# Kernel optimization log

Hardware: AMD Instinct MI355X
Metric: run time of the kernel (lower is better)

## Reference

```python
import jax, jax.numpy as jnp
import numpy as np

K = 64          # number of tags, incl. BOS/EOS
V = 50000       # vocab size (excl. BOS/EOS words)
D = 128         # lexicon embedding dim
BOS_T = K - 2   # BOS tag index
EOS_T = K - 1   # EOS tag index
BATCH = 8192
L = 126         # interior words per sentence (n = L + 2 incl. BOS/EOS)
EPS = 1e-45     # smoothing added to A and B in updateAB


def setup_inputs() -> dict:
    key = jax.random.key(0)
    k1, k2, k3, k4 = jax.random.split(key, 4)
    words = jax.random.randint(k1, (BATCH, L), 0, V, dtype=jnp.int32)
    ThetaB = 0.01 * jax.random.uniform(k2, (K, D), dtype=jnp.float32)
    WA = 0.01 * jax.random.uniform(k3, (K, K), dtype=jnp.float32)
    E = jax.random.normal(k4, (V, D), dtype=jnp.float32)
    return {"words": words, "ThetaB": ThetaB, "WA": WA, "E": E}


def reference(words, ThetaB, WA, E):
    # updateAB(): A = softmax(WA) with BOS column forced to prob 0 (-inf logit)
    WAm = WA.at[:, BOS_T].set(-jnp.inf)
    A = jax.nn.softmax(WAm, axis=1) + EPS                       # [K, K]
    B = jax.nn.softmax(ThetaB @ E.T, axis=1)                    # [K, V]
    B = B.at[EOS_T, :].set(0.0).at[BOS_T, :].set(0.0) + EPS
    logA = jnp.log(A)                                           # [K, K]
    logB = jnp.log(B)                                           # [K, V]

    # Emission log-probs gathered per token: [L, B, K]
    em = jnp.swapaxes(logB.T[words], 0, 1)

    # alpha_0: one-hot (in log space) at BOS tag
    alpha0 = jnp.full((words.shape[0], K), -jnp.inf, dtype=logA.dtype)
    alpha0 = alpha0.at[:, BOS_T].set(0.0)

    def step(alpha, e):
        # alpha: [B, K] over prev tags; logsumexp over prev tag axis
        new = jax.nn.logsumexp(alpha[:, :, None] + logA[None, :, :], axis=1) + e
        return new, None

    alpha, _ = jax.lax.scan(step, alpha0, em)
    # Final transition into EOS tag (no emission): log Z per sentence, [B]
    logZ = jax.nn.logsumexp(alpha + logA[None, :, EOS_T], axis=1)
    return logZ
```

## Files before the change

kernel.cpp:

```cpp
#include <hip/hip_runtime.h>
#include <hip/hip_bf16.h>
#include <math.h>


#define KT 64
#define VV 50000
#define DD 128
#define BOS_T 62
#define EOS_T 63
#define LLEN 126
#define EPSF 1e-45f
#define SCALE_F 65536.0f
#define LOG_TOTAL_SCALE (2016.0f * 0.6931471805599453f)
#define NBLK 782
#define PBLK 784
#define TPH 14
#define NPH 9

#define BTN_OFF   0
#define A_OFF     6400000
#define SUM_OFF   6416384
#define PART_OFF  6416640

typedef short short8 __attribute__((ext_vector_type(8)));
typedef float f32x4  __attribute__((ext_vector_type(4)));

union U8 { short8 v; unsigned u[4]; short s[8]; };

static __device__ inline unsigned short f2bf_u(float x) {
    __hip_bfloat16 h = __float2bfloat16(x);
    return *reinterpret_cast<unsigned short*>(&h);
}
static __device__ inline short f2bf(float x) { return (short)f2bf_u(x); }

#if __has_builtin(__builtin_amdgcn_cvt_pk_bf16_f32)
typedef __bf16 bf16x2 __attribute__((ext_vector_type(2)));
static __device__ inline unsigned pk2(float a, float b) {
    bf16x2 r = __builtin_amdgcn_cvt_pk_bf16_f32(a, b);
    return *reinterpret_cast<unsigned*>(&r);
}
#else
static __device__ inline unsigned pk2(float a, float b) {
    union { float f; unsigned u; } ua, ub;
    ua.f = a; ub.f = b;
    return ((ua.u + 0x8000u) >> 16) | ((ub.u + 0x8000u) & 0xFFFF0000u);
}
#endif
static __device__ inline float lo16(unsigned u) { union { unsigned i; float f; } c; c.i = u << 16;        return c.f; }
static __device__ inline float hi16(unsigned u) { union { unsigned i; float f; } c; c.i = u & 0xffff0000u; return c.f; }

#if __has_builtin(__builtin_amdgcn_global_load_lds)
#define GLLDS(gp, lbase)                                                        \
    __builtin_amdgcn_global_load_lds(                                           \
        (__attribute__((address_space(1))) void*)const_cast<unsigned short*>(gp),\
        (__attribute__((address_space(3))) void*)(lbase), 16, 0, 0)
#else
#define GLLDS(gp, lbase)                                                        \
    do { *(uint4*)((unsigned short*)(lbase) + (threadIdx.x & 63) * 8) =         \
             *(const uint4*)(gp); } while (0)
#endif

__global__ __launch_bounds__(256) void k_emit(const float* __restrict__ ThetaB,
                                              const float* __restrict__ E,
                                              unsigned short* __restrict__ btn_bf,
                                              float* __restrict__ partial) {
    __shared__ float red[4][KT];
    int t    = threadIdx.x;
    int lane = t & 63;
    int w    = t >> 6;
    int n    = lane & 15;
    int q    = lane >> 4;
    int v0   = (blockIdx.x * 4 + w) * 16;

    int rowE = v0 + n;
    bool valid = rowE < VV;
    rowE = valid ? rowE : VV - 1;
    float4 ex[4][2];
#pragma unroll
    for (int kt = 0; kt < 4; ++kt) {
        const float* p = E + (size_t)rowE * DD + kt * 32 + q * 8;
        ex[kt][0] = *(const float4*)p;
        ex[kt][1] = *(const float4*)(p + 4);
    }

    short8 Th[4][4];
#pragma unroll
    for (int kt = 0; kt < 4; ++kt)
#pragma unroll
        for (int mt = 0; mt < 4; ++mt) {
            const float* p = ThetaB + (mt * 16 + n) * DD + kt * 32 + q * 8;
            float4 x = *(const float4*)p;
            float4 y = *(const float4*)(p + 4);
            U8 f;
            f.u[0] = pk2(x.x, x.y); f.u[1] = pk2(x.z, x.w);
            f.u[2] = pk2(y.x, y.y); f.u[3] = pk2(y.z, y.w);
            Th[kt][mt] = f.v;
        }

    short8 Ef[4];
#pragma unroll
    for (int kt = 0; kt < 4; ++kt) {
        U8 f;
        f.u[0] = pk2(ex[kt][0].x, ex[kt][0].y); f.u[1] = pk2(ex[kt][0].z, ex[kt][0].w);
        f.u[2] = pk2(ex[kt][1].x, ex[kt][1].y); f.u[3] = pk2(ex[kt][1].z, ex[kt][1].w);
        Ef[kt] = f.v;
    }

#pragma unroll
    for (int mt = 0; mt < 4; ++mt) {
        f32x4 C = {0.f, 0.f, 0.f, 0.f};
#pragma unroll
        for (int kt = 0; kt < 4; ++kt)
            C = __builtin_amdgcn_mfma_f32_16x16x32_bf16(Th[kt][mt], Ef[kt], C, 0, 0, 0);
        float e[4];
#pragma unroll
        for (int r = 0; r < 4; ++r) e[r] = __expf(C[r]);
        if (valid) {
            uint2 st = make_uint2(pk2(e[0], e[1]), pk2(e[2], e[3]));
            *(uint2*)(btn_bf + (size_t)rowE * KT + mt * 16 + q * 4) = st;
        }
#pragma unroll
        for (int r = 0; r < 4; ++r) {
            float s = valid ? e[r] : 0.0f;
            s += __shfl_xor(s, 1, 64);
            s += __shfl_xor(s, 2, 64);
            s += __shfl_xor(s, 4, 64);
            s += __shfl_xor(s, 8, 64);
            if (n == 0) red[w][mt * 16 + q * 4 + r] = s;
        }
    }
    __syncthreads();
    if (w == 0) {
        float s = red[0][lane] + red[1][lane] + red[2][lane] + red[3][lane];
        partial[lane * PBLK + blockIdx.x] = s;
    }
}

__global__ __launch_bounds__(256) void k_sumA(const float* __restrict__ partial,
                                              const float* __restrict__ WA,
                                              float* __restrict__ sumexp,
                                              float* __restrict__ A) {
    __shared__ float r[4];
    int k = blockIdx.x;
    int t = threadIdx.x;
    float s = 0.0f;
    for (int i = t; i < NBLK; i += 256) s += partial[k * PBLK + i];
#pragma unroll
    for (int off = 32; off > 0; off >>= 1) s += __shfl_xor(s, off, 64);
    if ((t & 63) == 0) r[t >> 6] = s;
    __syncthreads();
    if (t == 0) sumexp[k] = r[0] + r[1] + r[2] + r[3];
    if (t < 64) {
        float wv = WA[k * KT + t];
        float e = (t == BOS_T) ? 0.0f : __expf(wv);
        float se = e;
#pragma unroll
        for (int off = 32; off > 0; off >>= 1) se += __shfl_xor(se, off, 64);
        A[k * KT + t] = e / se + EPSF;
    }
}

__global__ __launch_bounds__(64) void k_fwd(const int* __restrict__ words,
                                            const unsigned short* __restrict__ btn_bf,
                                            const float* __restrict__ A,
                                            const float* __restrict__ sumexp,
                                            float* __restrict__ out) {
    __shared__ int shw[16 * LLEN];
    __shared__ __attribute__((aligned(16))) unsigned short shE[2][TPH * 1024];
    int lane = threadIdx.x & 63;
    int n    = lane & 15;
    int qA   = lane >> 4;
    int b0   = blockIdx.x * 16;

    {
        const uint4* src = (const uint4*)(words + (size_t)b0 * LLEN);
        uint4* dst = (uint4*)shw;
#pragma unroll
        for (int i = 0; i < 8; ++i) {
            int idx = lane + 64 * i;
            if (idx < (16 * LLEN) / 4) dst[idx] = src[idx];
        }
    }

    short8 Af[2][4];
#pragma unroll
    for (int mt = 0; mt < 4; ++mt) {
        int tagn = 32 * (mt >> 1) + 8 * (n >> 2) + 4 * (mt & 1) + (n & 3);
        float s = sumexp[tagn];
        float rsn = (tagn == BOS_T || tagn == EOS_T) ? 0.0f : (SCALE_F / s);
#pragma unroll
        for (int kt = 0; kt < 2; ++kt) {
            U8 f;
#pragma unroll
            for (int j = 0; j < 8; ++j)
                f.s[j] = f2bf(A[(kt * 32 + qA * 8 + j) * KT + tagn] * rsn);
            Af[kt][mt] = f.v;
        }
    }

    short8 B0, B1;
    {
        U8 z; z.u[0] = z.u[1] = z.u[2] = z.u[3] = 0;
        B0 = z.v;
        U8 o; o.u[0] = o.u[1] = o.u[2] = o.u[3] = 0;
        if (qA == 3) o.s[6] = (short)0x3F80;
        B1 = o.v;
    }

#define STAGE(bb, t0)                                                        \
    do {                                                                     \
        _Pragma("unroll")                                                    \
        for (int s_ = 0; s_ < TPH; ++s_) {                                   \
            int wd_ = shw[n * LLEN + (t0) + s_];                             \
            const unsigned short* g_ = btn_bf + (size_t)wd_ * KT + qA * 8;   \
            GLLDS(g_, &shE[bb][s_ * 1024]);                                  \
            GLLDS(g_ + 32, &shE[bb][s_ * 1024 + 512]);                       \
        }                                                                    \
    } while (0)

#define LDE(bb, ss, hh) (*(const uint4*)(&shE[bb][(ss) * 1024 + (hh) * 512] + lane * 8))

    STAGE(0, 0);
    asm volatile("s_waitcnt vmcnt(0)" ::: "memory");

    for (int p = 0; p < NPH; ++p) {
        int b = p & 1;
        if (p + 1 < NPH) STAGE((p + 1) & 1, (p + 1) * TPH);

        uint4 a0 = LDE(b, 0, 0), a1 = LDE(b, 0, 1);
        uint4 c0 = LDE(b, 1, 0), c1 = LDE(b, 1, 1);
#pragma unroll
        for (int s = 0; s < TPH; ++s) {
            uint4 e0 = a0, e1 = a1;
            a0 = c0; a1 = c1;
            int s2 = (s + 2 < TPH) ? s + 2 : TPH - 1;
            c0 = LDE(b, s2, 0); c1 = LDE(b, s2, 1);

            f32x4 C[4];
#pragma unroll
            for (int mt = 0; mt < 4; ++mt) {
                f32x4 acc = {0.f, 0.f, 0.f, 0.f};
                acc = __builtin_amdgcn_mfma_f32_16x16x32_bf16(Af[0][mt], B0, acc, 0, 0, 0);
                acc = __builtin_amdgcn_mfma_f32_16x16x32_bf16(Af[1][mt], B1, acc, 0, 0, 0);
                C[mt] = acc;
            }
            U8 f0, f1;
            f0.u[0] = pk2(C[0][0] * lo16(e0.x), C[0][1] * hi16(e0.x));
            f0.u[1] = pk2(C[0][2] * lo16(e0.y), C[0][3] * hi16(e0.y));
            f0.u[2] = pk2(C[1][0] * lo16(e0.z), C[1][1] * hi16(e0.z));
            f0.u[3] = pk2(C[1][2] * lo16(e0.w), C[1][3] * hi16(e0.w));
            f1.u[0] = pk2(C[2][0] * lo16(e1.x), C[2][1] * hi16(e1.x));
            f1.u[1] = pk2(C[2][2] * lo16(e1.y), C[2][3] * hi16(e1.y));
            f1.u[2] = pk2(C[3][0] * lo16(e1.z), C[3][1] * hi16(e1.z));
            f1.u[3] = pk2(C[3][2] * lo16(e1.w), C[3][3] * hi16(e1.w));
            B0 = f0.v; B1 = f1.v;
        }
        asm volatile("s_waitcnt vmcnt(0)" ::: "memory");
    }

    short8 Afin[2];
#pragma unroll
    for (int kt = 0; kt < 2; ++kt) {
        U8 f;
#pragma unroll
        for (int j = 0; j < 8; ++j)
            f.s[j] = (n == 0) ? f2bf(A[(kt * 32 + qA * 8 + j) * KT + EOS_T]) : (short)0;
        Afin[kt] = f.v;
    }
    f32x4 Cf = {0.f, 0.f, 0.f, 0.f};
    Cf = __builtin_amdgcn_mfma_f32_16x16x32_bf16(Afin[0], B0, Cf, 0, 0, 0);
    Cf = __builtin_amdgcn_mfma_f32_16x16x32_bf16(Afin[1], B1, Cf, 0, 0, 0);
    if (qA == 0)
        out[b0 + n] = logf(Cf[0]) - LOG_TOTAL_SCALE;
}

extern "C" void kernel_launch(void* const* d_in, const int* in_sizes, int n_in,
                              void* d_out, int out_size, void* d_ws, size_t ws_size,
                              hipStream_t stream) {
    const int*   words  = (const int*)d_in[0];
    const float* ThetaB = (const float*)d_in[1];
    const float* WA     = (const float*)d_in[2];
    const float* E      = (const float*)d_in[3];
    float* out = (float*)d_out;

    char* ws = (char*)d_ws;
    unsigned short* btn_bf = (unsigned short*)(ws + BTN_OFF);
    float* A       = (float*)(ws + A_OFF);
    float* sumexp  = (float*)(ws + SUM_OFF);
    float* partial = (float*)(ws + PART_OFF);

    k_emit<<<NBLK, 256, 0, stream>>>(ThetaB, E, btn_bf, partial);
    k_sumA<<<KT, 256, 0, stream>>>(partial, WA, sumexp, A);
    k_fwd<<<8192 / 16, 64, 0, stream>>>(words, btn_bf, A, sumexp, out);
}
```

Measured before the change: 139.4 us.

## Warp-specialize forward kernel: three producer waves stage emissions, one wave computes

The forward kernel now runs 256 threads per block. Three waves gather emission rows from global memory into the LDS double buffer while the fourth wave runs the MFMA recurrence, and the phases are handed off with block barriers. This is meant to take the gather latency off the serial compute wave's critical path. In exchange the block is four times larger, which may reduce how many blocks fit per CU, and each phase now pays a __syncthreads.

```diff
diff --git a/kernel.cpp b/kernel.cpp
--- a/kernel.cpp
+++ b/kernel.cpp
@@ -160,14 +160,15 @@
     }
 }
 
-__global__ __launch_bounds__(64) void k_fwd(const int* __restrict__ words,
-                                            const unsigned short* __restrict__ btn_bf,
-                                            const float* __restrict__ A,
-                                            const float* __restrict__ sumexp,
-                                            float* __restrict__ out) {
+__global__ __launch_bounds__(256) void k_fwd(const int* __restrict__ words,
+                                             const unsigned short* __restrict__ btn_bf,
+                                             const float* __restrict__ A,
+                                             const float* __restrict__ sumexp,
+                                             float* __restrict__ out) {
     __shared__ int shw[16 * LLEN];
     __shared__ __attribute__((aligned(16))) unsigned short shE[2][TPH * 1024];
     int lane = threadIdx.x & 63;
+    int w    = threadIdx.x >> 6;
     int n    = lane & 15;
     int qA   = lane >> 4;
     int b0   = blockIdx.x * 16;
@@ -175,103 +176,104 @@
     {
         const uint4* src = (const uint4*)(words + (size_t)b0 * LLEN);
         uint4* dst = (uint4*)shw;
-#pragma unroll
-        for (int i = 0; i < 8; ++i) {
-            int idx = lane + 64 * i;
-            if (idx < (16 * LLEN) / 4) dst[idx] = src[idx];
-        }
+        for (int idx = threadIdx.x; idx < (16 * LLEN) / 4; idx += 256)
+            dst[idx] = src[idx];
     }
 
     short8 Af[2][4];
-#pragma unroll
-    for (int mt = 0; mt < 4; ++mt) {
-        int tagn = 32 * (mt >> 1) + 8 * (n >> 2) + 4 * (mt & 1) + (n & 3);
-        float s = sumexp[tagn];
-        float rsn = (tagn == BOS_T || tagn == EOS_T) ? 0.0f : (SCALE_F / s);
-#pragma unroll
-        for (int kt = 0; kt < 2; ++kt) {
-            U8 f;
-#pragma unroll
-            for (int j = 0; j < 8; ++j)
-                f.s[j] = f2bf(A[(kt * 32 + qA * 8 + j) * KT + tagn] * rsn);
-            Af[kt][mt] = f.v;
-        }
-    }
-
     short8 B0, B1;
-    {
+    if (w == 3) {
+#pragma unroll
+        for (int mt = 0; mt < 4; ++mt) {
+            int tagn = 32 * (mt >> 1) + 8 * (n >> 2) + 4 * (mt & 1) + (n & 3);
+            float s = sumexp[tagn];
+            float rsn = (tagn == BOS_T || tagn == EOS_T) ? 0.0f : (SCALE_F / s);
+#pragma unroll
+            for (int kt = 0; kt < 2; ++kt) {
+                U8 f;
+#pragma unroll
+                for (int j = 0; j < 8; ++j)
+                    f.s[j] = f2bf(A[(kt * 32 + qA * 8 + j) * KT + tagn] * rsn);
+                Af[kt][mt] = f.v;
+            }
+        }
         U8 z; z.u[0] = z.u[1] = z.u[2] = z.u[3] = 0;
         B0 = z.v;
         U8 o; o.u[0] = o.u[1] = o.u[2] = o.u[3] = 0;
         if (qA == 3) o.s[6] = (short)0x3F80;
         B1 = o.v;
     }
-
-#define STAGE(bb, t0)                                                        \
-    do {                                                                     \
-        _Pragma("unroll")                                                    \
-        for (int s_ = 0; s_ < TPH; ++s_) {                                   \
-            int wd_ = shw[n * LLEN + (t0) + s_];                             \
-            const unsigned short* g_ = btn_bf + (size_t)wd_ * KT + qA * 8;   \
-            GLLDS(g_, &shE[bb][s_ * 1024]);                                  \
-            GLLDS(g_ + 32, &shE[bb][s_ * 1024 + 512]);                       \
-        }                                                                    \
+    __syncthreads();
+
+#define PSTAGE(bb, p_)                                                        \
+    do {                                                                      \
+        for (int s_ = w; s_ < TPH; s_ += 3) {                                 \
+            int wd_ = shw[n * LLEN + (p_) * TPH + s_];                        \
+            const unsigned short* g_ = btn_bf + (size_t)wd_ * KT + qA * 8;    \
+            GLLDS(g_, &shE[bb][s_ * 1024]);                                   \
+            GLLDS(g_ + 32, &shE[bb][s_ * 1024 + 512]);                        \
+        }                                                                     \
+        asm volatile("s_waitcnt vmcnt(0)" ::: "memory");                      \
     } while (0)
 
 #define LDE(bb, ss, hh) (*(const uint4*)(&shE[bb][(ss) * 1024 + (hh) * 512] + lane * 8))
 
-    STAGE(0, 0);
-    asm volatile("s_waitcnt vmcnt(0)" ::: "memory");
+    if (w < 3) PSTAGE(0, 0);
+    __syncthreads();
 
     for (int p = 0; p < NPH; ++p) {
         int b = p & 1;
-        if (p + 1 < NPH) STAGE((p + 1) & 1, (p + 1) * TPH);
-
-        uint4 a0 = LDE(b, 0, 0), a1 = LDE(b, 0, 1);
-        uint4 c0 = LDE(b, 1, 0), c1 = LDE(b, 1, 1);
-#pragma unroll
-        for (int s = 0; s < TPH; ++s) {
-            uint4 e0 = a0, e1 = a1;
-            a0 = c0; a1 = c1;
-            int s2 = (s + 2 < TPH) ? s + 2 : TPH - 1;
-            c0 = LDE(b, s2, 0); c1 = LDE(b, s2, 1);
-
-            f32x4 C[4];
-#pragma unroll
-            for (int mt = 0; mt < 4; ++mt) {
-                f32x4 acc = {0.f, 0.f, 0.f, 0.f};
-                acc = __builtin_amdgcn_mfma_f32_16x16x32_bf16(Af[0][mt], B0, acc, 0, 0, 0);
-                acc = __builtin_amdgcn_mfma_f32_16x16x32_bf16(Af[1][mt], B1, acc, 0, 0, 0);
-                C[mt] = acc;
+        if (w < 3) {
+            if (p + 1 < NPH) PSTAGE((p + 1) & 1, p + 1);
+        } else {
+            uint4 a0 = LDE(b, 0, 0), a1 = LDE(b, 0, 1);
+            uint4 c0 = LDE(b, 1, 0), c1 = LDE(b, 1, 1);
+#pragma unroll
+            for (int s = 0; s < TPH; ++s) {
+                uint4 e0 = a0, e1 = a1;
+                a0 = c0; a1 = c1;
+                int s2 = (s + 2 < TPH) ? s + 2 : TPH - 1;
+                c0 = LDE(b, s2, 0); c1 = LDE(b, s2, 1);
+
+                f32x4 C[4];
+#pragma unroll
+                for (int mt = 0; mt < 4; ++mt) {
+                    f32x4 acc = {0.f, 0.f, 0.f, 0.f};
+                    acc = __builtin_amdgcn_mfma_f32_16x16x32_bf16(Af[0][mt], B0, acc, 0, 0, 0);
+                    acc = __builtin_amdgcn_mfma_f32_16x16x32_bf16(Af[1][mt], B1, acc, 0, 0, 0);
+                    C[mt] = acc;
+                }
+                U8 f0, f1;
+                f0.u[0] = pk2(C[0][0] * lo16(e0.x), C[0][1] * hi16(e0.x));
+                f0.u[1] = pk2(C[0][2] * lo16(e0.y), C[0][3] * hi16(e0.y));
+                f0.u[2] = pk2(C[1][0] * lo16(e0.z), C[1][1] * hi16(e0.z));
+                f0.u[3] = pk2(C[1][2] * lo16(e0.w), C[1][3] * hi16(e0.w));
+                f1.u[0] = pk2(C[2][0] * lo16(e1.x), C[2][1] * hi16(e1.x));
+                f1.u[1] = pk2(C[2][2] * lo16(e1.y), C[2][3] * hi16(e1.y));
+                f1.u[2] = pk2(C[3][0] * lo16(e1.z), C[3][1] * hi16(e1.z));
+                f1.u[3] = pk2(C[3][2] * lo16(e1.w), C[3][3] * hi16(e1.w));
+                B0 = f0.v; B1 = f1.v;
             }
-            U8 f0, f1;
-            f0.u[0] = pk2(C[0][0] * lo16(e0.x), C[0][1] * hi16(e0.x));
-            f0.u[1] = pk2(C[0][2] * lo16(e0.y), C[0][3] * hi16(e0.y));
-            f0.u[2] = pk2(C[1][0] * lo16(e0.z), C[1][1] * hi16(e0.z));
-            f0.u[3] = pk2(C[1][2] * lo16(e0.w), C[1][3] * hi16(e0.w));
-            f1.u[0] = pk2(C[2][0] * lo16(e1.x), C[2][1] * hi16(e1.x));
-            f1.u[1] = pk2(C[2][2] * lo16(e1.y), C[2][3] * hi16(e1.y));
-            f1.u[2] = pk2(C[3][0] * lo16(e1.z), C[3][1] * hi16(e1.z));
-            f1.u[3] = pk2(C[3][2] * lo16(e1.w), C[3][3] * hi16(e1.w));
-            B0 = f0.v; B1 = f1.v;
-        }
-        asm volatile("s_waitcnt vmcnt(0)" ::: "memory");
-    }
-
-    short8 Afin[2];
-#pragma unroll
-    for (int kt = 0; kt < 2; ++kt) {
-        U8 f;
-#pragma unroll
-        for (int j = 0; j < 8; ++j)
-            f.s[j] = (n == 0) ? f2bf(A[(kt * 32 + qA * 8 + j) * KT + EOS_T]) : (short)0;
-        Afin[kt] = f.v;
-    }
-    f32x4 Cf = {0.f, 0.f, 0.f, 0.f};
-    Cf = __builtin_amdgcn_mfma_f32_16x16x32_bf16(Afin[0], B0, Cf, 0, 0, 0);
-    Cf = __builtin_amdgcn_mfma_f32_16x16x32_bf16(Afin[1], B1, Cf, 0, 0, 0);
-    if (qA == 0)
-        out[b0 + n] = logf(Cf[0]) - LOG_TOTAL_SCALE;
+        }
+        __syncthreads();
+    }
+
+    if (w == 3) {
+        short8 Afin[2];
+#pragma unroll
+        for (int kt = 0; kt < 2; ++kt) {
+            U8 f;
+#pragma unroll
+            for (int j = 0; j < 8; ++j)
+                f.s[j] = (n == 0) ? f2bf(A[(kt * 32 + qA * 8 + j) * KT + EOS_T]) : (short)0;
+            Afin[kt] = f.v;
+        }
+        f32x4 Cf = {0.f, 0.f, 0.f, 0.f};
+        Cf = __builtin_amdgcn_mfma_f32_16x16x32_bf16(Afin[0], B0, Cf, 0, 0, 0);
+        Cf = __builtin_amdgcn_mfma_f32_16x16x32_bf16(Afin[1], B1, Cf, 0, 0, 0);
+        if (qA == 0)
+            out[b0 + n] = logf(Cf[0]) - LOG_TOTAL_SCALE;
+    }
 }
 
 extern "C" void kernel_launch(void* const* d_in, const int* in_sizes, int n_in,
@@ -291,5 +293,5 @@
 
     k_emit<<<NBLK, 256, 0, stream>>>(ThetaB, E, btn_bf, partial);
     k_sumA<<<KT, 256, 0, stream>>>(partial, WA, sumexp, A);
-    k_fwd<<<8192 / 16, 64, 0, stream>>>(words, btn_bf, A, sumexp, out);
-}
+    k_fwd<<<8192 / 16, 256, 0, stream>>>(words, btn_bf, A, sumexp, out);
+}
```

After: 129.8 us. 6.9% less time.
